# Kernel tuning notes

Measured on AMD Instinct MI355X. Metric: run time of the kernel, lower is better.

Reference implementation:

```python
import jax, jax.numpy as jnp
import numpy as np

B, S_SRC, S_TGT = 4096, 32, 32
V_SRC, V_TGT, E, H = 96, 128, 128, 512
SOS = 1


def _lstm_cell(h, c, x, Wih, Whh, bih, bhh):
    # PyTorch LSTM gate layout: [i, f, g, o] along 4H
    gates = x @ Wih.T + bih + h @ Whh.T + bhh  # (B, 4H)
    i, f, g, o = jnp.split(gates, 4, axis=-1)
    i, f, o = jax.nn.sigmoid(i), jax.nn.sigmoid(f), jax.nn.sigmoid(o)
    g = jnp.tanh(g)
    c2 = f * c + i * g
    h2 = o * jnp.tanh(c2)
    return h2, c2


def setup_inputs() -> dict:
    key = jax.random.key(0)
    ks = jax.random.split(key, 16)
    u = lambda k, shp, s: jax.random.uniform(k, shp, jnp.float32, -s, s)
    sh = 1.0 / np.sqrt(H)
    emb_src = u(ks[0], (V_SRC, E), 0.1).at[0].set(0.0)  # padding_idx=0
    emb_tgt = u(ks[1], (V_TGT, E), 0.1).at[0].set(0.0)
    inp = {
        "src_seq": jax.random.randint(ks[2], (B, S_SRC), 1, V_SRC),
        "src_lengths": jax.random.randint(ks[3], (B,), 1, S_SRC + 1),
        "tgt_seq": jax.random.randint(ks[4], (B, S_TGT), 1, V_TGT),
        "emb_src": emb_src,
        "enc_Wih": u(ks[5], (4 * H, E), sh),
        "enc_Whh": u(ks[6], (4 * H, H), sh),
        "enc_bih": u(ks[7], (4 * H,), sh),
        "enc_bhh": u(ks[8], (4 * H,), sh),
        "emb_tgt": emb_tgt,
        "dec_Wih": u(ks[9], (4 * H, E), sh),
        "dec_Whh": u(ks[10], (4 * H, H), sh),
        "dec_bih": u(ks[11], (4 * H,), sh),
        "dec_bhh": u(ks[12], (4 * H,), sh),
        "W_out": u(ks[13], (V_TGT, H), sh),
        "b_out": u(ks[14], (V_TGT,), sh),
    }
    return inp


def reference(src_seq, src_lengths, tgt_seq,
              emb_src, enc_Wih, enc_Whh, enc_bih, enc_bhh,
              emb_tgt, dec_Wih, dec_Whh, dec_bih, dec_bhh,
              W_out, b_out):
    batch = src_seq.shape[0]
    h0 = jnp.zeros((batch, H), jnp.float32)
    c0 = jnp.zeros((batch, H), jnp.float32)

    # ---- Encoder: masked LSTM == pack_padded_sequence semantics ----
    x_src = emb_src[src_seq]                                # (B, S, E)
    x_src_t = jnp.swapaxes(x_src, 0, 1)                     # (S, B, E)
    mask = (jnp.arange(S_SRC)[:, None] < src_lengths[None, :])[:, :, None]  # (S,B,1)

    def enc_step(carry, inp):
        h, c = carry
        x, m = inp
        h2, c2 = _lstm_cell(h, c, x, enc_Wih, enc_Whh, enc_bih, enc_bhh)
        h = jnp.where(m, h2, h)
        c = jnp.where(m, c2, c)
        return (h, c), None

    (h_enc, c_enc), _ = jax.lax.scan(enc_step, (h0, c0), (x_src_t, mask))

    # ---- Decoder: full teacher forcing (ratio=1.0), eval-mode dropout ----
    dec_in = jnp.concatenate(
        [jnp.full((batch, 1), SOS, tgt_seq.dtype), tgt_seq[:, :-1]], axis=1)  # (B, T)
    x_tgt_t = jnp.swapaxes(emb_tgt[dec_in], 0, 1)           # (T, B, E)

    def dec_step(carry, x):
        h, c = carry
        h2, c2 = _lstm_cell(h, c, x, dec_Wih, dec_Whh, dec_bih, dec_bhh)
        return (h2, c2), h2

    _, hs = jax.lax.scan(dec_step, (h_enc, c_enc), x_tgt_t)  # (T, B, H)

    logits = jnp.einsum('tbh,vh->btv', hs, W_out) + b_out    # (B, T, V_TGT)
    return logits
```

## Files before the change

### kernel.cpp

```cpp
#include <hip/hip_runtime.h>
#include <hip/hip_bf16.h>
#include <hip/hip_fp16.h>
#include <stdint.h>


#define NB     4096
#define SSRC   32
#define STGT   32
#define NVSRC  96
#define NVTGT  128
#define ED     128
#define HD     512
#define G4     2048
#define NBHD   ((size_t)NB * HD)

typedef __attribute__((ext_vector_type(8))) _Float16 half8;
typedef __attribute__((ext_vector_type(4))) float fx4;

#define AS_G __attribute__((address_space(1)))
#define AS_L __attribute__((address_space(3)))

__device__ __forceinline__ void gl2lds16(const void* g, void* l) {
    __builtin_amdgcn_global_load_lds((const AS_G uint32_t*)g, (AS_L uint32_t*)l, 16, 0, 0);
}

__device__ __forceinline__ float sigf(float x) { return 1.0f / (1.0f + __expf(-x)); }
__device__ __forceinline__ float tanhfast(float x) { return 1.0f - 2.0f / (__expf(2.0f * x) + 1.0f); }

__global__ void convert_half(const float* __restrict__ src, int n, _Float16* __restrict__ dst) {
    int i = blockIdx.x * 256 + threadIdx.x;
    if (i < n) dst[i] = (_Float16)src[i];
}

__global__ __launch_bounds__(256) void transpose_f32(
    const float* __restrict__ in, float* __restrict__ outT, int R, int C, int rtiles)
{
    __shared__ float ls[32][33];
    const int bx = (int)blockIdx.x % rtiles;
    const int by = (int)blockIdx.x / rtiles;
    const int tx = threadIdx.x & 31, ty = threadIdx.x >> 5;
    #pragma unroll
    for (int i = 0; i < 4; i++) {
        int rr = ty + i * 8;
        ls[rr][tx] = in[(size_t)(bx * 32 + rr) * C + by * 32 + tx];
    }
    __syncthreads();
    #pragma unroll
    for (int i = 0; i < 4; i++) {
        int rr = ty + i * 8;
        outT[(size_t)(by * 32 + rr) * R + bx * 32 + tx] = ls[tx][rr];
    }
}

__global__ __launch_bounds__(256) void build_tables3(
    const float* __restrict__ emb, const float* __restrict__ WT,
    const float* __restrict__ bih, const float* __restrict__ bhh,
    float* __restrict__ proj)
{
    __shared__ float embL[8][ED];
    const int gc = (int)blockIdx.x & 7;
    const int vc = (int)blockIdx.x >> 3;
    const int g  = gc * 256 + threadIdx.x;
    for (int i = threadIdx.x; i < 8 * ED; i += 256)
        embL[i >> 7][i & (ED - 1)] = emb[(size_t)(vc * 8 + (i >> 7)) * ED + (i & (ED - 1))];
    __syncthreads();
    float acc[8] = {0, 0, 0, 0, 0, 0, 0, 0};
    for (int e = 0; e < ED; e++) {
        float w = WT[(size_t)e * G4 + g];
        #pragma unroll
        for (int v = 0; v < 8; v++) acc[v] += embL[v][e] * w;
    }
    float bb = bih[g] + bhh[g];
    #pragma unroll
    for (int v = 0; v < 8; v++)
        proj[(size_t)(vc * 8 + v) * G4 + g] = acc[v] + bb;
}

__global__ __launch_bounds__(256, 4) void lstm_step(
    const _Float16* __restrict__ h_r, _Float16* __restrict__ h_w,
    float* __restrict__ c_state,
    const float* __restrict__ proj,
    const int* __restrict__ seq, const int* __restrict__ lens,
    const _Float16* __restrict__ W,
    int t, int is_enc, int skip_gemm)
{
    __shared__ __align__(16) _Float16 lsA[128 * 64];
    __shared__ __align__(16) _Float16 lsB[64 * 64];

    const int tid = threadIdx.x;
    const int lane = tid & 63;
    const int wid  = tid >> 6;
    const int srow = lane >> 3;
    const int skc  = (((lane & 7) ^ srow)) << 3;
    const int wm   = wid * 32;
    const int quad = lane >> 4;
    const int l15  = lane & 15;

    const int x = (int)blockIdx.x & 7, j = (int)blockIdx.x >> 3;
    const int m0 = ((x & 1) * 16 + (j & 15)) * 128;
    const int c0 = ((x >> 1) * 8 + (j >> 4)) * 16;

    const _Float16 *ag[4], *bg[2];
    #pragma unroll
    for (int i = 0; i < 4; i++) {
        int lr = wid * 32 + i * 8 + srow;
        ag[i] = h_r + (size_t)(m0 + lr) * HD + skc;
    }
    #pragma unroll
    for (int i = 0; i < 2; i++) {
        int lr = wid * 16 + i * 8 + srow;
        int wr = (lr >> 4) * HD + c0 + (lr & 15);
        bg[i] = W + (size_t)wr * HD + skc;
    }

    fx4 acc[2][4];
    #pragma unroll
    for (int i = 0; i < 2; i++)
        #pragma unroll
        for (int jj = 0; jj < 4; jj++)
            acc[i][jj] = fx4{0.f, 0.f, 0.f, 0.f};

    if (!skip_gemm) {
        for (int k0 = 0; k0 < HD; k0 += 64) {
            __syncthreads();
            #pragma unroll
            for (int i = 0; i < 4; i++)
                gl2lds16(ag[i] + k0, &lsA[(wid * 32 + i * 8) * 64]);
            #pragma unroll
            for (int i = 0; i < 2; i++)
                gl2lds16(bg[i] + k0, &lsB[(wid * 16 + i * 8) * 64]);
            __syncthreads();
            #pragma unroll
            for (int kk = 0; kk < 64; kk += 32) {
                const int kc = (kk >> 3) + quad;
                half8 af[2], bf[4];
                #pragma unroll
                for (int mf = 0; mf < 2; mf++) {
                    int ar = wm + mf * 16 + l15;
                    int sw = ((kc ^ (ar & 7)) << 3);
                    af[mf] = *(const half8*)&lsA[ar * 64 + sw];
                }
                #pragma unroll
                for (int g = 0; g < 4; g++) {
                    int br = g * 16 + l15;
                    int sw = ((kc ^ (br & 7)) << 3);
                    bf[g] = *(const half8*)&lsB[br * 64 + sw];
                }
                #pragma unroll
                for (int mf = 0; mf < 2; mf++)
                    #pragma unroll
                    for (int g = 0; g < 4; g++)
                        acc[mf][g] = __builtin_amdgcn_mfma_f32_16x16x32_f16(af[mf], bf[g], acc[mf][g], 0, 0, 0);
            }
        }
    }

    const int hcol = c0 + l15;
    #pragma unroll
    for (int mf = 0; mf < 2; mf++) {
        #pragma unroll
        for (int r = 0; r < 4; r++) {
            int row = m0 + wm + mf * 16 + quad * 4 + r;
            int tok = is_enc ? seq[row * SSRC + t]
                             : (t == 0 ? 1 : seq[row * STGT + t - 1]);
            const float* xp = proj + (size_t)tok * G4 + hcol;
            float gi = acc[mf][0][r] + xp[0];
            float gf = acc[mf][1][r] + xp[HD];
            float gg = acc[mf][2][r] + xp[2 * HD];
            float go = acc[mf][3][r] + xp[3 * HD];
            float ii = sigf(gi), ff = sigf(gf), oo = sigf(go);
            float g2 = tanhfast(gg);
            size_t off = (size_t)row * HD + hcol;
            float cold = c_state[off];
            float c2 = ff * cold + ii * g2;
            float h2 = oo * tanhfast(c2);
            if (is_enc && t >= lens[row]) {
                c2 = cold;
                h2 = (float)h_r[off];
            }
            c_state[off] = c2;
            h_w[off] = (_Float16)h2;
        }
    }
}

__global__ __launch_bounds__(256, 2) void outproj_batch(
    const _Float16* __restrict__ h_slots, int t0,
    const _Float16* __restrict__ Wo, const float* __restrict__ bout,
    float* __restrict__ out)
{
    __shared__ __align__(16) _Float16 lsA[128 * 64];
    __shared__ __align__(16) _Float16 lsB[128 * 64];

    const int tid = threadIdx.x;
    const int lane = tid & 63;
    const int wid  = tid >> 6;
    const int srow = lane >> 3;
    const int skc  = (((lane & 7) ^ srow)) << 3;
    const int wm    = (wid >> 1) * 64;
    const int wncol = wid & 1;
    const int quad  = lane >> 4;
    const int l15   = lane & 15;
    const int bsw   = (l15 & 7);

    const int t  = t0 + ((int)blockIdx.x >> 5);
    const int m0 = ((int)blockIdx.x & 31) * 128;
    const _Float16* h_r = h_slots + (size_t)(t % 10) * NBHD;

    const _Float16 *ag[4], *bg[4];
    #pragma unroll
    for (int i = 0; i < 4; i++) {
        int lr = wid * 32 + i * 8 + srow;
        ag[i] = h_r + (size_t)(m0 + lr) * HD + skc;
        bg[i] = Wo + (size_t)lr * HD + skc;
    }

    fx4 acc[4][4];
    #pragma unroll
    for (int i = 0; i < 4; i++)
        #pragma unroll
        for (int jj = 0; jj < 4; jj++)
            acc[i][jj] = fx4{0.f, 0.f, 0.f, 0.f};

    for (int k0 = 0; k0 < HD; k0 += 64) {
        __syncthreads();
        #pragma unroll
        for (int i = 0; i < 4; i++) {
            int lb = (wid * 32 + i * 8) * 64;
            gl2lds16(ag[i] + k0, &lsA[lb]);
            gl2lds16(bg[i] + k0, &lsB[lb]);
        }
        __syncthreads();
        #pragma unroll
        for (int kk = 0; kk < 64; kk += 32) {
            const int kc = (kk >> 3) + quad;
            const int sw = ((kc ^ bsw) << 3);
            half8 af[4], bf[4];
            #pragma unroll
            for (int mt = 0; mt < 4; mt++)
                af[mt] = *(const half8*)&lsA[(wm + mt * 16 + l15) * 64 + sw];
            #pragma unroll
            for (int nt = 0; nt < 4; nt++)
                bf[nt] = *(const half8*)&lsB[(wncol * 64 + nt * 16 + l15) * 64 + sw];
            #pragma unroll
            for (int mt = 0; mt < 4; mt++)
                #pragma unroll
                for (int nt = 0; nt < 4; nt++)
                    acc[mt][nt] = __builtin_amdgcn_mfma_f32_16x16x32_f16(af[mt], bf[nt], acc[mt][nt], 0, 0, 0);
        }
    }

    #pragma unroll
    for (int mt = 0; mt < 4; mt++)
        #pragma unroll
        for (int nt = 0; nt < 4; nt++) {
            int v = wncol * 64 + nt * 16 + l15;
            float bo = bout[v];
            #pragma unroll
            for (int r = 0; r < 4; r++) {
                int row = m0 + wm + mt * 16 + quad * 4 + r;
                out[((size_t)row * STGT + t) * NVTGT + v] = acc[mt][nt][r] + bo;
            }
        }
}

extern "C" void kernel_launch(void* const* d_in, const int* in_sizes, int n_in,
                              void* d_out, int out_size, void* d_ws, size_t ws_size,
                              hipStream_t stream) {
    (void)in_sizes; (void)n_in; (void)out_size; (void)ws_size;
    const int* src_seq = (const int*)d_in[0];
    const int* src_len = (const int*)d_in[1];
    const int* tgt_seq = (const int*)d_in[2];
    const float* emb_src = (const float*)d_in[3];
    const float* eWih = (const float*)d_in[4];
    const float* eWhh = (const float*)d_in[5];
    const float* ebih = (const float*)d_in[6];
    const float* ebhh = (const float*)d_in[7];
    const float* emb_tgt = (const float*)d_in[8];
    const float* dWih = (const float*)d_in[9];
    const float* dWhh = (const float*)d_in[10];
    const float* dbih = (const float*)d_in[11];
    const float* dbhh = (const float*)d_in[12];
    const float* Wout = (const float*)d_in[13];
    const float* bout = (const float*)d_in[14];
    float* out = (float*)d_out;

    char* ws = (char*)d_ws;
    size_t off = 0;
    auto carve = [&](size_t bytes) { void* p = ws + off; off += (bytes + 255) & ~(size_t)255; return p; };
    float* proj_src = (float*)carve((size_t)NVSRC * G4 * 4);
    float* proj_tgt = (float*)carve((size_t)NVTGT * G4 * 4);
    float* c_state  = (float*)carve(NBHD * 4);
    _Float16* slots = (_Float16*)carve((size_t)12 * NBHD * 2);
    _Float16* eW_h  = (_Float16*)carve((size_t)G4 * HD * 2);
    _Float16* dW_h  = (_Float16*)carve((size_t)G4 * HD * 2);
    _Float16* Wo_h  = (_Float16*)carve((size_t)NVTGT * HD * 2);
    float* WT_e = (float*)(slots);
    float* WT_d = (float*)((char*)slots + (size_t)ED * G4 * 4);
    auto slot = [&](int i) { return slots + (size_t)i * NBHD; };

    hipMemsetAsync(c_state, 0, NBHD * 4, stream);
    hipMemsetAsync(slot(10), 0, NBHD * 2, stream);

    convert_half<<<dim3(G4 * HD / 256), dim3(256), 0, stream>>>(eWhh, G4 * HD, eW_h);
    convert_half<<<dim3(G4 * HD / 256), dim3(256), 0, stream>>>(dWhh, G4 * HD, dW_h);
    convert_half<<<dim3(NVTGT * HD / 256), dim3(256), 0, stream>>>(Wout, NVTGT * HD, Wo_h);
    transpose_f32<<<dim3((G4 / 32) * (ED / 32)), dim3(256), 0, stream>>>(eWih, WT_e, G4, ED, G4 / 32);
    transpose_f32<<<dim3((G4 / 32) * (ED / 32)), dim3(256), 0, stream>>>(dWih, WT_d, G4, ED, G4 / 32);
    build_tables3<<<dim3((NVSRC / 8) * 8), dim3(256), 0, stream>>>(emb_src, WT_e, ebih, ebhh, proj_src);
    build_tables3<<<dim3((NVTGT / 8) * 8), dim3(256), 0, stream>>>(emb_tgt, WT_d, dbih, dbhh, proj_tgt);

    for (int s = 0; s < 32; s++) {
        lstm_step<<<dim3(1024), dim3(256), 0, stream>>>(
            slot(10 + (s & 1)), slot(10 + ((s + 1) & 1)), c_state,
            proj_src, src_seq, src_len, eW_h, s, 1, (s == 0));
    }
    for (int t = 0; t < 32; t++) {
        const _Float16* hr = (t == 0) ? slot(10) : slot((t - 1) % 10);
        lstm_step<<<dim3(1024), dim3(256), 0, stream>>>(
            hr, slot(t % 10), c_state,
            proj_tgt, tgt_seq, nullptr, dW_h, t, 0, 0);
        if ((t & 7) == 7) {
            outproj_batch<<<dim3(256), dim3(256), 0, stream>>>(
                slots, t - 7, Wo_h, bout, out);
        }
    }
}
```

Before: 1.558 ms.

## Double-buffer the hidden-state tile with prefetch and vmcnt-based waits in the LSTM GEMM

Result: slower. 1.596 ms (+2.4%).

```diff
diff --git a/kernel.cpp b/kernel.cpp
--- a/kernel.cpp
+++ b/kernel.cpp
@@ -84,7 +84,7 @@
     const _Float16* __restrict__ W,
     int t, int is_enc, int skip_gemm)
 {
-    __shared__ __align__(16) _Float16 lsA[128 * 64];
+    __shared__ __align__(16) _Float16 lsA[2][128 * 64];
     __shared__ __align__(16) _Float16 lsB[64 * 64];
 
     const int tid = threadIdx.x;
@@ -121,15 +121,24 @@
             acc[i][jj] = fx4{0.f, 0.f, 0.f, 0.f};
 
     if (!skip_gemm) {
-        for (int k0 = 0; k0 < HD; k0 += 64) {
-            __syncthreads();
-            #pragma unroll
-            for (int i = 0; i < 4; i++)
-                gl2lds16(ag[i] + k0, &lsA[(wid * 32 + i * 8) * 64]);
-            #pragma unroll
-            for (int i = 0; i < 2; i++)
-                gl2lds16(bg[i] + k0, &lsB[(wid * 16 + i * 8) * 64]);
-            __syncthreads();
+        #pragma unroll
+        for (int i = 0; i < 2; i++)
+            gl2lds16(bg[i], &lsB[(wid * 16 + i * 8) * 64]);
+        #pragma unroll
+        for (int i = 0; i < 4; i++)
+            gl2lds16(ag[i], &lsA[0][(wid * 32 + i * 8) * 64]);
+        #pragma unroll
+        for (int i = 0; i < 4; i++)
+            gl2lds16(ag[i] + 64, &lsA[1][(wid * 32 + i * 8) * 64]);
+
+        #pragma unroll
+        for (int it = 0; it < 8; it++) {
+            if (it < 7) asm volatile("s_waitcnt vmcnt(4)" ::: "memory");
+            else        asm volatile("s_waitcnt vmcnt(0)" ::: "memory");
+            __builtin_amdgcn_s_barrier();
+            __builtin_amdgcn_sched_barrier(0);
+            const _Float16* la = lsA[it & 1];
+            __builtin_amdgcn_s_setprio(1);
             #pragma unroll
             for (int kk = 0; kk < 64; kk += 32) {
                 const int kc = (kk >> 3) + quad;
@@ -138,7 +147,7 @@
                 for (int mf = 0; mf < 2; mf++) {
                     int ar = wm + mf * 16 + l15;
                     int sw = ((kc ^ (ar & 7)) << 3);
-                    af[mf] = *(const half8*)&lsA[ar * 64 + sw];
+                    af[mf] = *(const half8*)&la[ar * 64 + sw];
                 }
                 #pragma unroll
                 for (int g = 0; g < 4; g++) {
@@ -150,7 +159,21 @@
                 for (int mf = 0; mf < 2; mf++)
                     #pragma unroll
                     for (int g = 0; g < 4; g++)
-                        acc[mf][g] = __builtin_amdgcn_mfma_f32_16x16x32_f16(af[mf], bf[g], acc[mf][g], 0, 0, 0);
+                        acc[mf][g] = __builtin_amdgcn_mfma_f32_16x16x32_f16(
+                            af[mf], bf[g], acc[mf][g], 0, 0, 0);
+            }
+            __builtin_amdgcn_s_setprio(0);
+            if (it < 7) {
+                __builtin_amdgcn_sched_barrier(0);
+                __builtin_amdgcn_s_barrier();
+                #pragma unroll
+                for (int i = 0; i < 2; i++)
+                    gl2lds16(bg[i] + (it + 1) * 64, &lsB[(wid * 16 + i * 8) * 64]);
+                if (it + 2 < 8) {
+                    #pragma unroll
+                    for (int i = 0; i < 4; i++)
+                        gl2lds16(ag[i] + (it + 2) * 64, &lsA[it & 1][(wid * 32 + i * 8) * 64]);
+                }
             }
         }
     }
```

## Sort batch rows by source length and skip finished encoder tiles

Applied to the files above, without the earlier changes.

Measured after the change: 1.458 ms. -6.4%, faster.

```diff
diff --git a/kernel.cpp b/kernel.cpp
--- a/kernel.cpp
+++ b/kernel.cpp
@@ -71,17 +71,55 @@
         for (int v = 0; v < 8; v++) acc[v] += embL[v][e] * w;
     }
     float bb = bih[g] + bhh[g];
+    const int gate = g >> 9, hcol = g & (HD - 1);
     #pragma unroll
     for (int v = 0; v < 8; v++)
-        proj[(size_t)(vc * 8 + v) * G4 + g] = acc[v] + bb;
+        proj[(((size_t)(vc * 8 + v) * HD + hcol) << 2) + gate] = acc[v] + bb;
+}
+
+__global__ __launch_bounds__(256) void sort_rows(
+    const int* __restrict__ lens, int* __restrict__ perm,
+    int* __restrict__ lens_s, int* __restrict__ maxlen)
+{
+    __shared__ int hist[33];
+    __shared__ int base[33];
+    const int tid = threadIdx.x;
+    if (tid < 33) hist[tid] = 0;
+    __syncthreads();
+    for (int i = tid; i < NB; i += 256) atomicAdd(&hist[lens[i]], 1);
+    __syncthreads();
+    if (tid == 0) {
+        int s = 0;
+        for (int l = 1; l <= 32; l++) { base[l] = s; s += hist[l]; }
+    }
+    __syncthreads();
+    for (int i = tid; i < NB; i += 256) {
+        int l = lens[i];
+        int pos = atomicAdd(&base[l], 1);
+        perm[pos] = i;
+        lens_s[pos] = l;
+    }
+    __syncthreads();
+    if (tid < 32) maxlen[tid] = lens_s[tid * 128 + 127];
+}
+
+__global__ __launch_bounds__(256) void gather_seq(
+    const int* __restrict__ seq, const int* __restrict__ perm,
+    int* __restrict__ seq_s)
+{
+    int i = (int)blockIdx.x * 256 + threadIdx.x;
+    int row = i >> 5, t = i & 31;
+    seq_s[i] = seq[perm[row] * 32 + t];
 }
 
 __global__ __launch_bounds__(256, 4) void lstm_step(
     const _Float16* __restrict__ h_r, _Float16* __restrict__ h_w,
     float* __restrict__ c_state,
     const float* __restrict__ proj,
-    const int* __restrict__ seq, const int* __restrict__ lens,
+    const int* __restrict__ seq_s, const int* __restrict__ lens_s,
+    const int* __restrict__ maxlen,
     const _Float16* __restrict__ W,
+    _Float16* __restrict__ hfinal,
     int t, int is_enc, int skip_gemm)
 {
     __shared__ __align__(16) _Float16 lsA[128 * 64];
@@ -97,8 +135,11 @@
     const int l15  = lane & 15;
 
     const int x = (int)blockIdx.x & 7, j = (int)blockIdx.x >> 3;
-    const int m0 = ((x & 1) * 16 + (j & 15)) * 128;
+    const int mt = (x & 1) * 16 + (j & 15);
+    const int m0 = mt * 128;
     const int c0 = ((x >> 1) * 8 + (j >> 4)) * 16;
+
+    if (is_enc && t >= maxlen[mt]) return;
 
     const _Float16 *ag[4], *bg[2];
     #pragma unroll
@@ -161,22 +202,27 @@
         #pragma unroll
         for (int r = 0; r < 4; r++) {
             int row = m0 + wm + mf * 16 + quad * 4 + r;
-            int tok = is_enc ? seq[row * SSRC + t]
-                             : (t == 0 ? 1 : seq[row * STGT + t - 1]);
-            const float* xp = proj + (size_t)tok * G4 + hcol;
+            int tok = is_enc ? seq_s[row * SSRC + t]
+                             : (t == 0 ? 1 : seq_s[row * STGT + t - 1]);
+            const fx4 xp = *(const fx4*)&proj[((size_t)tok * HD + hcol) << 2];
             float gi = acc[mf][0][r] + xp[0];
-            float gf = acc[mf][1][r] + xp[HD];
-            float gg = acc[mf][2][r] + xp[2 * HD];
-            float go = acc[mf][3][r] + xp[3 * HD];
+            float gf = acc[mf][1][r] + xp[1];
+            float gg = acc[mf][2][r] + xp[2];
+            float go = acc[mf][3][r] + xp[3];
             float ii = sigf(gi), ff = sigf(gf), oo = sigf(go);
             float g2 = tanhfast(gg);
             size_t off = (size_t)row * HD + hcol;
             float cold = c_state[off];
             float c2 = ff * cold + ii * g2;
             float h2 = oo * tanhfast(c2);
-            if (is_enc && t >= lens[row]) {
-                c2 = cold;
-                h2 = (float)h_r[off];
+            if (is_enc) {
+                int len = lens_s[row];
+                if (t >= len) {
+                    c2 = cold;
+                    h2 = (float)h_r[off];
+                }
+                if (t + 1 == len)
+                    hfinal[off] = (_Float16)h2;
             }
             c_state[off] = c2;
             h_w[off] = (_Float16)h2;
@@ -187,6 +233,7 @@
 __global__ __launch_bounds__(256, 2) void outproj_batch(
     const _Float16* __restrict__ h_slots, int t0,
     const _Float16* __restrict__ Wo, const float* __restrict__ bout,
+    const int* __restrict__ perm,
     float* __restrict__ out)
 {
     __shared__ __align__(16) _Float16 lsA[128 * 64];
@@ -259,7 +306,8 @@
             #pragma unroll
             for (int r = 0; r < 4; r++) {
                 int row = m0 + wm + mt * 16 + quad * 4 + r;
-                out[((size_t)row * STGT + t) * NVTGT + v] = acc[mt][nt][r] + bo;
+                int orow = perm[row];
+                out[((size_t)orow * STGT + t) * NVTGT + v] = acc[mt][nt][r] + bo;
             }
         }
 }
@@ -295,12 +343,21 @@
     _Float16* eW_h  = (_Float16*)carve((size_t)G4 * HD * 2);
     _Float16* dW_h  = (_Float16*)carve((size_t)G4 * HD * 2);
     _Float16* Wo_h  = (_Float16*)carve((size_t)NVTGT * HD * 2);
+    _Float16* hfinal = (_Float16*)carve(NBHD * 2);
+    int* perm   = (int*)carve((size_t)NB * 4);
+    int* lens_s = (int*)carve((size_t)NB * 4);
+    int* maxlen = (int*)carve(32 * 4);
+    int* src_s  = (int*)carve((size_t)NB * SSRC * 4);
+    int* tgt_s  = (int*)carve((size_t)NB * STGT * 4);
     float* WT_e = (float*)(slots);
     float* WT_d = (float*)((char*)slots + (size_t)ED * G4 * 4);
     auto slot = [&](int i) { return slots + (size_t)i * NBHD; };
 
     hipMemsetAsync(c_state, 0, NBHD * 4, stream);
-    hipMemsetAsync(slot(10), 0, NBHD * 2, stream);
+
+    sort_rows<<<dim3(1), dim3(256), 0, stream>>>(src_len, perm, lens_s, maxlen);
+    gather_seq<<<dim3(NB * SSRC / 256), dim3(256), 0, stream>>>(src_seq, perm, src_s);
+    gather_seq<<<dim3(NB * STGT / 256), dim3(256), 0, stream>>>(tgt_seq, perm, tgt_s);
 
     convert_half<<<dim3(G4 * HD / 256), dim3(256), 0, stream>>>(eWhh, G4 * HD, eW_h);
     convert_half<<<dim3(G4 * HD / 256), dim3(256), 0, stream>>>(dWhh, G4 * HD, dW_h);
@@ -313,16 +370,16 @@
     for (int s = 0; s < 32; s++) {
         lstm_step<<<dim3(1024), dim3(256), 0, stream>>>(
             slot(10 + (s & 1)), slot(10 + ((s + 1) & 1)), c_state,
-            proj_src, src_seq, src_len, eW_h, s, 1, (s == 0));
+            proj_src, src_s, lens_s, maxlen, eW_h, hfinal, s, 1, (s == 0));
     }
     for (int t = 0; t < 32; t++) {
-        const _Float16* hr = (t == 0) ? slot(10) : slot((t - 1) % 10);
+        const _Float16* hr = (t == 0) ? hfinal : slot((t - 1) % 10);
         lstm_step<<<dim3(1024), dim3(256), 0, stream>>>(
             hr, slot(t % 10), c_state,
-            proj_tgt, tgt_seq, nullptr, dW_h, t, 0, 0);
+            proj_tgt, tgt_s, lens_s, maxlen, dW_h, hfinal, t, 0, 0);
         if ((t & 7) == 7) {
             outproj_batch<<<dim3(256), dim3(256), 0, stream>>>(
-                slots, t - 7, Wo_h, bout, out);
-        }
-    }
-}
+                slots, t - 7, Wo_h, bout, perm, out);
+        }
+    }
+}
```
